# Kernel tuning notes

Measured on AMD Instinct MI355X. Metric: run time of the kernel, lower is better.

## Reference

```python
import jax, jax.numpy as jnp
import numpy as np

B, T_PREFIX, C_IN = 8, 6144, 8
OUT_LEN, OUT_C = 2048, 8
AUX_DIM = 16
D_MODEL, D_STATE, HEADDIM, EXPAND = 256, 32, 64, 2
D_INNER = EXPAND * D_MODEL            # 512
NHEADS = D_INNER // HEADDIM           # 8
CONV_DIM = D_INNER + 2 * D_STATE      # 576
D_PROJ = 2 * D_INNER + 2 * D_STATE + NHEADS  # 1096
N_LAYERS = 2
CHUNK = 64
PATCH = 16
PRECONV_K = 5
DCONV_K = 4


def setup_inputs() -> dict:
    key = jax.random.key(0)
    ks = iter(jax.random.split(key, 64))
    def rn(shape, s=0.02):
        return s * jax.random.normal(next(ks), shape, jnp.float32)
    inp = dict(
        x_prefix=jax.random.normal(next(ks), (B, T_PREFIX, C_IN), jnp.float32),
        y_aux=jax.random.normal(next(ks), (B, AUX_DIM), jnp.float32),
        pre_conv_w=rn((D_MODEL, C_IN, PRECONV_K), 0.1),
        pre_conv_b=rn((D_MODEL,)),
        patch_w=rn((D_MODEL, D_MODEL, PATCH), 0.05),
        patch_b=rn((D_MODEL,)),
        mask_token=rn((D_MODEL,)),
        aux_w=rn((AUX_DIM, D_MODEL), 0.1),
        aux_b=rn((D_MODEL,)),
        patch_out_w=rn((2 * D_MODEL, OUT_C * PATCH), 0.05),
        patch_out_b=rn((OUT_C * PATCH,)),
    )
    for d in ('fwd', 'bwd'):
        inp[f'{d}_norm_w'] = jnp.ones((N_LAYERS, D_MODEL), jnp.float32)
        inp[f'{d}_inproj'] = rn((N_LAYERS, D_MODEL, D_PROJ), 0.05)
        inp[f'{d}_conv_w'] = rn((N_LAYERS, CONV_DIM, DCONV_K), 0.2)
        inp[f'{d}_conv_b'] = rn((N_LAYERS, CONV_DIM))
        inp[f'{d}_dtbias'] = rn((N_LAYERS, NHEADS), 0.5)
        inp[f'{d}_Alog'] = jnp.tile(jnp.log(jnp.arange(1, NHEADS + 1, dtype=jnp.float32)), (N_LAYERS, 1))
        inp[f'{d}_D'] = jnp.ones((N_LAYERS, NHEADS), jnp.float32)
        inp[f'{d}_gnorm'] = jnp.ones((N_LAYERS, D_INNER), jnp.float32)
        inp[f'{d}_outproj'] = rn((N_LAYERS, D_INNER, D_MODEL), 0.05)
    return inp


def rmsnorm(x, w, eps=1e-5):
    return x * jax.lax.rsqrt(jnp.mean(x * x, axis=-1, keepdims=True) + eps) * w


def conv1d(x, w, b, stride, pad):  # x: [B,C,T], w: [O,I,K]
    y = jax.lax.conv_general_dilated(x, w, (stride,), [(pad, pad)],
                                     dimension_numbers=('NCH', 'OIH', 'NCH'))
    return y + b[None, :, None]


def mamba_block(u, inproj, conv_w, conv_b, dtbias, Alog, Dp, gnorm_w, outproj):
    # Mamba-2/SSD style block: in_proj -> z | xBC | dt, causal depthwise conv,
    # selective scan with per-head scalar decay A, +D skip, gated RMSNorm, out_proj.
    b, T, _ = u.shape
    zxbcdt = u @ inproj                                   # [b,T,D_PROJ]
    z = zxbcdt[..., :D_INNER]
    xBC = zxbcdt[..., D_INNER:D_INNER + CONV_DIM]
    dt = jax.nn.softplus(zxbcdt[..., -NHEADS:] + dtbias)  # [b,T,H]
    # causal depthwise conv over time
    xc = jax.lax.conv_general_dilated(xBC.transpose(0, 2, 1), conv_w[:, None, :], (1,),
                                      [(DCONV_K - 1, 0)],
                                      dimension_numbers=('NCH', 'OIH', 'NCH'),
                                      feature_group_count=CONV_DIM)
    xBC = jax.nn.silu((xc + conv_b[None, :, None]).transpose(0, 2, 1))
    xs = xBC[..., :D_INNER].reshape(b, T, NHEADS, HEADDIM)  # [b,T,H,P]
    Bm = xBC[..., D_INNER:D_INNER + D_STATE]                # [b,T,N]
    Cm = xBC[..., D_INNER + D_STATE:]                       # [b,T,N]
    A = -jnp.exp(Alog)                                      # [H]

    def step(h, inps):  # h: [b,H,P,N]
        dt_t, x_t, B_t, C_t = inps
        dA = jnp.exp(dt_t * A)[:, :, None, None]
        h = h * dA + (dt_t[:, :, None] * x_t)[..., None] * B_t[:, None, None, :]
        y = jnp.einsum('bhpn,bn->bhp', h, C_t)
        return h, y

    h0 = jnp.zeros((b, NHEADS, HEADDIM, D_STATE), u.dtype)
    _, ys = jax.lax.scan(step, h0, (dt.transpose(1, 0, 2), xs.transpose(1, 0, 2, 3),
                                    Bm.transpose(1, 0, 2), Cm.transpose(1, 0, 2)))
    y = ys.transpose(1, 0, 2, 3) + Dp[None, None, :, None] * xs
    y = y.reshape(b, T, D_INNER)
    y = rmsnorm(y * jax.nn.silu(z), gnorm_w)
    return y @ outproj


def reference(x_prefix, y_aux, pre_conv_w, pre_conv_b, patch_w, patch_b, mask_token,
              aux_w, aux_b, fwd_norm_w, fwd_inproj, fwd_conv_w, fwd_conv_b, fwd_dtbias,
              fwd_Alog, fwd_D, fwd_gnorm, fwd_outproj, bwd_norm_w, bwd_inproj,
              bwd_conv_w, bwd_conv_b, bwd_dtbias, bwd_Alog, bwd_D, bwd_gnorm,
              bwd_outproj, patch_out_w, patch_out_b):
    b = x_prefix.shape[0]
    t_total = T_PREFIX + OUT_LEN
    x_full = jnp.pad(x_prefix, ((0, 0), (0, OUT_LEN), (0, 0)))        # zeros for future
    x = jax.nn.silu(conv1d(x_full.transpose(0, 2, 1), pre_conv_w, pre_conv_b, 1, PRECONV_K // 2))
    x = conv1d(x, patch_w, patch_b, PATCH, 0).transpose(0, 2, 1)      # [b, n_tokens, d_model]
    n_tokens = x.shape[1]
    # eval mode: deterministic future-patch mask, dropout is identity
    starts = jnp.arange(n_tokens) * PATCH
    mask = (starts >= T_PREFIX)[None, :, None]
    x = jnp.where(mask, mask_token[None, None, :], x)
    aux_bias = jax.nn.silu(y_aux @ aux_w + aux_b)[:, None, :]
    x = x + aux_bias
    pad_t = (-n_tokens) % CHUNK
    if pad_t:
        x = jnp.pad(x, ((0, 0), (0, pad_t), (0, 0)))
    h_f = x
    h_b = x[:, ::-1]
    for i in range(N_LAYERS):
        h_f = h_f + mamba_block(rmsnorm(h_f, fwd_norm_w[i]), fwd_inproj[i], fwd_conv_w[i],
                                fwd_conv_b[i], fwd_dtbias[i], fwd_Alog[i], fwd_D[i],
                                fwd_gnorm[i], fwd_outproj[i])
        h_b = h_b + mamba_block(rmsnorm(h_b, bwd_norm_w[i]), bwd_inproj[i], bwd_conv_w[i],
                                bwd_conv_b[i], bwd_dtbias[i], bwd_Alog[i], bwd_D[i],
                                bwd_gnorm[i], bwd_outproj[i])
    h = jnp.concatenate([h_f, h_b[:, ::-1]], axis=-1)[:, :n_tokens]   # [b,n,2*d_model]
    patch_pred = h @ patch_out_w + patch_out_b                        # [b,n,out_c*patch]
    y = patch_pred.reshape(b, n_tokens, OUT_C, PATCH).reshape(b, n_tokens * PATCH, OUT_C)
    y = y[:, :t_total, :]
    return y[:, T_PREFIX:, :]
```

## Files before the change

### kernel.cpp

```cpp
#include <hip/hip_runtime.h>
#include <hip/hip_bf16.h>
#include <math.h>

#define BSZ      8
#define TPREF    6144
#define CIN      8
#define DMODEL   256
#define DINNER   512
#define DSTATE   32
#define NHEADS   8
#define HEADDIM  64
#define CONVDIM  576
#define DPROJ    1096
#define NTOK     512
#define NVIS     384
#define TBWD     128
#define MFWD     (BSZ * NTOK)
#define MBWD     (BSZ * TBWD)
#define MALL     (MFWD + MBWD)

typedef float f32x4 __attribute__((ext_vector_type(4)));
typedef __bf16 bf16x8 __attribute__((ext_vector_type(8)));

__device__ __forceinline__ float silu_f(float x) { return x / (1.f + expf(-x)); }
// ... 26 lines not shown
        #pragma unroll
        for (int i = 0; i < 2; i++) {
            int s = i * 256 + tid;
            ASYNC16(A + (size_t)(m0 + (s >> 2)) * K + kb + (s & 3) * 8, sm + s * 16);
        }
        #pragma unroll
        for (int i = 0; i < 2; i++) {
            int s = i * 256 + tid;
            ASYNC16(Bt + (size_t)(n0 + (s >> 2)) * K + kb + (s & 3) * 8, sm + 8192 + s * 16);
        }
        __syncthreads();
        bf16x8 af[4], bfr[4];
        #pragma unroll
        for (int mf = 0; mf < 4; mf++)
            af[mf] = *(const bf16x8*)(sm + (wm * 64 + mf * 16 + lm) * 64 + q * 16);
        #pragma unroll
        for (int nf = 0; nf < 4; nf++)
            bfr[nf] = *(const bf16x8*)(sm + 8192 + (wn * 64 + nf * 16 + lm) * 64 + q * 16);
        #pragma unroll
        for (int mf = 0; mf < 4; mf++)
            #pragma unroll
            for (int nf = 0; nf < 4; nf++)
                acc[mf][nf] = __builtin_amdgcn_mfma_f32_16x16x32_bf16(af[mf], bfr[nf], acc[mf][nf], 0, 0, 0);
        __syncthreads();
    }

    #pragma unroll
    for (int mf = 0; mf < 4; mf++) {
        int mbase = m0 + wm * 64 + mf * 16 + q * 4;
        #pragma unroll
        for (int nf = 0; nf < 4; nf++) {
            int n = n0 + wn * 64 + nf * 16 + lm;
            if (n < N) {
                #pragma unroll
                for (int r = 0; r < 4; r++) {
                    float v = acc[mf][nf][r];
                    size_t ci = (size_t)(mbase + r) * ldc + n;
                    if (flags & 4) {
                        v = silu_f(v + bias[n]);
                        ((__bf16*)C)[ci] = (__bf16)v;
                    } else if (flags & 8) {
                        C[ci + (size_t)blockIdx.z * pstr] = v;
                    } else if (flags & 2) {
                        atomicAdd(C + ci, v);
                    } else {
                        C[ci] = v;
                    }
                }
            }
        }
    }
}

__global__ __launch_bounds__(256) void gemm_inproj_norm(
    const float* __restrict__ h, const float* __restrict__ wnf, const float* __restrict__ wnb,
    const __bf16* __restrict__ ipTf, const __bf16* __restrict__ ipTb,
    float* __restrict__ C) {
    __shared__ __bf16 Asm[128][264];
    __shared__ char Bsm[8192];
    int tid = threadIdx.x;
    int m0 = blockIdx.y * 128, n0 = blockIdx.x * 128;
    int dir = (m0 >= MFWD);
    const float* wnorm = dir ? wnb : wnf;
    const __bf16* Bt = dir ? ipTb : ipTf;
    {
        int row = tid >> 1, half = tid & 1;
        const float4* xr = (const float4*)(h + (size_t)(m0 + row) * 256 + half * 128);
        const float4* wr = (const float4*)(wnorm + half * 128);
        float ss = 0.f;
        #pragma unroll
        for (int c = 0; c < 32; c++) {
            float4 v = xr[c], wv = wr[c];
            ss += v.x * v.x + v.y * v.y + v.z * v.z + v.w * v.w;
            __bf16 t4b[4] = {(__bf16)(v.x * wv.x), (__bf16)(v.y * wv.y),
                             (__bf16)(v.z * wv.z), (__bf16)(v.w * wv.w)};
            *(uint2*)&Asm[row][half * 128 + c * 4] = *(uint2*)t4b;
        }
        ss += __shfl_xor(ss, 1);
        float rs = rsqrtf(ss * (1.f / 256.f) + 1e-5f);
        #pragma unroll
        for (int c = 0; c < 16; c++) {
            union { uint4 u; __bf16 hh[8]; } a;
            a.u = *(uint4*)&Asm[row][half * 128 + c * 8];
            #pragma unroll
            for (int j = 0; j < 8; j++) a.hh[j] = (__bf16)((float)a.hh[j] * rs);
            *(uint4*)&Asm[row][half * 128 + c * 8] = a.u;
        }
    }
    __syncthreads();
    int w = tid >> 6, l = tid & 63;
    int wm = w >> 1, wn_ = w & 1, lm = l & 15, q = l >> 4;
    f32x4 acc[4][4];
    #pragma unroll
    for (int i = 0; i < 4; i++)
        #pragma unroll
        for (int j = 0; j < 4; j++) acc[i][j] = (f32x4)0.f;
    for (int k0 = 0; k0 < 256; k0 += 32) {
        #pragma unroll
        for (int i = 0; i < 2; i++) {
            int s = i * 256 + tid;
            ASYNC16(Bt + (size_t)(n0 + (s >> 2)) * 256 + k0 + (s & 3) * 8, Bsm + s * 16);
        }
        __syncthreads();
        bf16x8 af[4], bfr[4];
        #pragma unroll
        for (int mf = 0; mf < 4; mf++)
            af[mf] = *(const bf16x8*)&Asm[wm * 64 + mf * 16 + lm][k0 + q * 8];
        #pragma unroll
        for (int nf = 0; nf < 4; nf++)
            bfr[nf] = *(const bf16x8*)(Bsm + (wn_ * 64 + nf * 16 + lm) * 64 + q * 16);
        #pragma unroll
        for (int mf = 0; mf < 4; mf++)
            #pragma unroll
            for (int nf = 0; nf < 4; nf++)
                acc[mf][nf] = __builtin_amdgcn_mfma_f32_16x16x32_bf16(af[mf], bfr[nf], acc[mf][nf], 0, 0, 0);
        __syncthreads();
    }
    #pragma unroll
    for (int mf = 0; mf < 4; mf++) {
        int mbase = m0 + wm * 64 + mf * 16 + q * 4;
        #pragma unroll
        for (int nf = 0; nf < 4; nf++) {
            int n = n0 + wn_ * 64 + nf * 16 + lm;
            if (n < DPROJ) {
                #pragma unroll
                for (int r = 0; r < 4; r++)
                    C[(size_t)(mbase + r) * DPROJ + n] = acc[mf][nf][r];
            }
        }
    }
}

__global__ __launch_bounds__(256) void gemm_outproj_gated(
    const __bf16* __restrict__ ysD, const float* __restrict__ zx,
    const float* __restrict__ gwf, const float* __restrict__ gwb,
    const __bf16* __restrict__ opTf, const __bf16* __restrict__ opTb,
    float* __restrict__ C) {
    __shared__ __bf16 Asm[64][520];
    __shared__ char Bsm[8192];
    int tid = threadIdx.x;
    int m0 = blockIdx.y * 64, n0 = blockIdx.x * 128;
    int dir = (m0 >= MFWD);
    const float* gw = dir ? gwb : gwf;
    const __bf16* Bt = dir ? opTb : opTf;
    {
        int row = tid >> 2, part = tid & 3;
        size_t gm = m0 + row;
        const uint4* yr = (const uint4*)(ysD + gm * 512 + part * 128);
        const float4* zr = (const float4*)(zx + gm * DPROJ + part * 128);
        const float4* gr = (const float4*)(gw + part * 128);
        float ss = 0.f;
        #pragma unroll
        for (int c = 0; c < 16; c++) {
            union { uint4 u; __bf16 hh[8]; } yv; yv.u = yr[c];
            float4 z0 = zr[c * 2], z1 = zr[c * 2 + 1];
            float4 g0 = gr[c * 2], g1 = gr[c * 2 + 1];
            float gg[8];
            gg[0] = (float)yv.hh[0] * silu_f(z0.x);
            gg[1] = (float)yv.hh[1] * silu_f(z0.y);
            gg[2] = (float)yv.hh[2] * silu_f(z0.z);
            gg[3] = (float)yv.hh[3] * silu_f(z0.w);
            gg[4] = (float)yv.hh[4] * silu_f(z1.x);
            gg[5] = (float)yv.hh[5] * silu_f(z1.y);
            gg[6] = (float)yv.hh[6] * silu_f(z1.z);
            gg[7] = (float)yv.hh[7] * silu_f(z1.w);
            #pragma unroll
            for (int j = 0; j < 8; j++) ss += gg[j] * gg[j];
            union { uint4 u; __bf16 hh[8]; } d;
            d.hh[0] = (__bf16)(gg[0] * g0.x); d.hh[1] = (__bf16)(gg[1] * g0.y);
            d.hh[2] = (__bf16)(gg[2] * g0.z); d.hh[3] = (__bf16)(gg[3] * g0.w);
            d.hh[4] = (__bf16)(gg[4] * g1.x); d.hh[5] = (__bf16)(gg[5] * g1.y);
            d.hh[6] = (__bf16)(gg[6] * g1.z); d.hh[7] = (__bf16)(gg[7] * g1.w);
            *(uint4*)&Asm[row][part * 128 + c * 8] = d.u;
        }
        ss += __shfl_xor(ss, 1);
        ss += __shfl_xor(ss, 2);
        float rs = rsqrtf(ss * (1.f / 512.f) + 1e-5f);
        #pragma unroll
        for (int c = 0; c < 16; c++) {
            union { uint4 u; __bf16 hh[8]; } a;
            a.u = *(uint4*)&Asm[row][part * 128 + c * 8];
            #pragma unroll
            for (int j = 0; j < 8; j++) a.hh[j] = (__bf16)((float)a.hh[j] * rs);
            *(uint4*)&Asm[row][part * 128 + c * 8] = a.u;
        }
    }
    __syncthreads();
    int w = tid >> 6, l = tid & 63;
    int wm = w >> 1, wn_ = w & 1, lm = l & 15, q = l >> 4;
    f32x4 acc[2][4];
    #pragma unroll
    for (int i = 0; i < 2; i++)
        #pragma unroll
        for (int j = 0; j < 4; j++) acc[i][j] = (f32x4)0.f;
    for (int k0 = 0; k0 < 512; k0 += 32) {
        #pragma unroll
        for (int i = 0; i < 2; i++) {
            int s = i * 256 + tid;
            ASYNC16(Bt + (size_t)(n0 + (s >> 2)) * 512 + k0 + (s & 3) * 8, Bsm + s * 16);
        }
        __syncthreads();
        bf16x8 af[2], bfr[4];
        #pragma unroll
        for (int mf = 0; mf < 2; mf++)
            af[mf] = *(const bf16x8*)&Asm[wm * 32 + mf * 16 + lm][k0 + q * 8];
        #pragma unroll
        for (int nf = 0; nf < 4; nf++)
            bfr[nf] = *(const bf16x8*)(Bsm + (wn_ * 64 + nf * 16 + lm) * 64 + q * 16);
        #pragma unroll
        for (int mf = 0; mf < 2; mf++)
            #pragma unroll
            for (int nf = 0; nf < 4; nf++)
                acc[mf][nf] = __builtin_amdgcn_mfma_f32_16x16x32_bf16(af[mf], bfr[nf], acc[mf][nf], 0, 0, 0);
        __syncthreads();
    }
    #pragma unroll
    for (int mf = 0; mf < 2; mf++) {
        int mbase = m0 + wm * 32 + mf * 16 + q * 4;
        #pragma unroll
        for (int nf = 0; nf < 4; nf++) {
            int n = n0 + wn_ * 64 + nf * 16 + lm;
            #pragma unroll
            for (int r = 0; r < 4; r++) {
                size_t ci = (size_t)(mbase + r) * DMODEL + n;
                C[ci] += acc[mf][nf][r];
            }
        }
    }
}

__global__ void prep_all(const float* __restrict__ pre_conv_w, const float* __restrict__ patch_w,
                         const float* __restrict__ ip0, const float* __restrict__ ip1,
                         const float* __restrict__ op0, const float* __restrict__ op1,
                         const float* __restrict__ pow_, const float* __restrict__ pob,
                         const float* __restrict__ y_aux, const float* __restrict__ aux_w,
                         const float* __restrict__ aux_b, const float* __restrict__ xp,
                         __bf16* __restrict__ WpreT, __bf16* __restrict__ WtT,
                         __bf16* __restrict__ inprojT, __bf16* __restrict__ outprojT,
                         __bf16* __restrict__ poT, float* __restrict__ auxb,
                         float* __restrict__ dout, __bf16* __restrict__ Aim) {
    __shared__ float tile[32][33];
    int bx = blockIdx.x, tid = threadIdx.x;
    int tx = tid & 31, ty = tid >> 5;
    if (bx < 256) {
        int o = bx, c = tid;
        float f[16];
        const float4* s = (const float4*)(patch_w + (size_t)o * 4096 + c * 16);
        #pragma unroll
        for (int j = 0; j < 4; j++) *(float4*)&f[j * 4] = s[j];
        #pragma unroll
        for (int k = 0; k < 16; k++)
            WtT[(size_t)o * 4096 + k * 256 + c] = (__bf16)f[k];
        return;
    }
    bx -= 256;
    if (bx < 1152) {
        int seg = bx / 288, rem = bx % 288;
        int n0 = (rem / 8) * 32, k0 = (rem % 8) * 32;
        const float* src = (seg < 2 ? ip0 : ip1) + (size_t)(seg & 1) * 256 * DPROJ;
        #pragma unroll
        for (int j = 0; j < 4; j++) {
            int r = ty + j * 8;
            int n = n0 + tx;
            tile[r][tx] = (n < DPROJ) ? src[(size_t)(k0 + r) * DPROJ + n] : 0.f;
        }
        __syncthreads();
        __bf16* dst = inprojT + (size_t)seg * 1152 * 256;
        #pragma unroll
        for (int j = 0; j < 4; j++) {
            int r = ty + j * 8;
            dst[(size_t)(n0 + r) * 256 + k0 + tx] = (__bf16)tile[tx][r];
        }
        return;
    }
    bx -= 1152;
    if (bx < 512) {
        int s = bx / 128, rem = bx % 128;
        int n0 = (rem / 16) * 32, k0 = (rem % 16) * 32;
        const float* src = (s < 2 ? op0 : op1) + (size_t)(s & 1) * DINNER * DMODEL;
        #pragma unroll
        for (int j = 0; j < 4; j++) {
// ... 92 lines not shown
__global__ __launch_bounds__(256) void dwconv2_kernel(
    const float* __restrict__ zx, const float* __restrict__ cwf, const float* __restrict__ cbf,
    const float* __restrict__ cwb, const float* __restrict__ cbb,
    __bf16* __restrict__ XtF, __bf16* __restrict__ XtB,
    __bf16* __restrict__ BCF, __bf16* __restrict__ BCB) {
    int cg = blockIdx.x;
    int id = blockIdx.y;
    int b, t0, T; size_t rowbase;
    const float *cw, *cb; __bf16 *Xt, *BC;
    if (id < 64) { b = id >> 3; t0 = (id & 7) * 64; T = NTOK; rowbase = (size_t)b * NTOK;
                   cw = cwf; cb = cbf; Xt = XtF; BC = BCF; }
    else { int i2 = id - 64; b = i2 >> 1; t0 = (i2 & 1) * 64; T = TBWD;
           rowbase = (size_t)MFWD + (size_t)b * TBWD; cw = cwb; cb = cbb; Xt = XtB; BC = BCB; }
    int c0 = cg * 64;
    __shared__ float xs[67][65];
    int lane = threadIdx.x & 63, grp = threadIdx.x >> 6;
    for (int r = grp; r < 67; r += 4) {
        int t = t0 - 3 + r;
        xs[r][lane] = (t >= 0) ? zx[(rowbase + t) * DPROJ + DINNER + c0 + lane] : 0.f;
    }
    __syncthreads();
    if (cg < 8) {
        int t = lane;
        #pragma unroll
        for (int ci = grp; ci < 64; ci += 4) {
            int c = c0 + ci;
            float acc = cb[c];
            #pragma unroll
            for (int k = 0; k < 4; k++) acc += cw[c * 4 + k] * xs[t + k][ci];
            Xt[((size_t)((b * 8 + cg) * 64 + ci)) * T + t0 + t] = (__bf16)silu_f(acc);
        }
    } else {
        int c = lane;
        #pragma unroll
        for (int ti = grp; ti < 64; ti += 4) {
            float acc = cb[c0 + c];
            #pragma unroll
            for (int k = 0; k < 4; k++) acc += cw[(c0 + c) * 4 + k] * xs[ti + k][c];
            BC[((size_t)(b * T + t0 + ti)) * 64 + c] = (__bf16)silu_f(acc);
        }
    }
}

__global__ __launch_bounds__(64) void scan_local(
    const __bf16* __restrict__ XtF, const __bf16* __restrict__ XtB,
    const __bf16* __restrict__ BCF, const __bf16* __restrict__ BCB,
    const float* __restrict__ zx,
    const float* __restrict__ dtbf, const float* __restrict__ dtbb,
    const float* __restrict__ Alogf, const float* __restrict__ Alogb,
    const float* __restrict__ Dpf, const float* __restrict__ Dpb,
    __bf16* __restrict__ ysD,
    __bf16* __restrict__ ChatF, __bf16* __restrict__ ChatB,
    float* __restrict__ dSF, float* __restrict__ dSB,
    float* __restrict__ DcsF, float* __restrict__ DcsB) {
    int id = blockIdx.x, hd = blockIdx.y;
    int b, c, T, NC; size_t rowbase;
    const __bf16 *Xt, *BC; __bf16* Chat; float *dS, *Dcs;
    const float *dtb, *Alog, *Dp;
    if (id < 64) { b = id >> 3; c = id & 7; T = NTOK; NC = 8; rowbase = (size_t)b * NTOK;
                   Xt = XtF; BC = BCF; Chat = ChatF; dS = dSF; Dcs = DcsF;
                   dtb = dtbf; Alog = Alogf; Dp = Dpf; }
    else { int i2 = id - 64; b = i2 >> 1; c = i2 & 1; T = TBWD; NC = 2;
           rowbase = (size_t)MFWD + (size_t)b * TBWD;
           Xt = XtB; BC = BCB; Chat = ChatB; dS = dSB; Dcs = DcsB;
           dtb = dtbb; Alog = Alogb; Dp = Dpb; }
    int bh = b * 8 + hd;
    int t0 = c * 64;
    int lane = threadIdx.x;
    int lm = lane & 15, q = lane >> 4;
    float A = -expf(Alog[hd]);
    float Dh = Dp[hd];

    __shared__ __bf16 Xl[64][72];
    __shared__ __bf16 BCl[64][72];
    __shared__ __bf16 Pl[64][72];
    __shared__ __bf16 Wbl[32][72];
    __shared__ float lcs[64], dts[64];

    const uint4* xg = (const uint4*)(Xt + (size_t)(bh * 64 + lane) * T + t0);
    const uint4* bg = (const uint4*)(BC + ((size_t)(b * T + t0 + lane)) * 64);
    uint4 xv[8], bv[8];
    #pragma unroll
    for (int k = 0; k < 8; k++) { xv[k] = xg[k]; bv[k] = bg[k]; }
    float xdt = zx[(rowbase + t0 + lane) * DPROJ + 1088 + hd] + dtb[hd];
    float dtv = (xdt > 20.f) ? xdt : log1pf(expf(xdt));
    #pragma unroll
    for (int k = 0; k < 8; k++) {
        *(uint4*)&Xl[lane][k * 8] = xv[k];
        *(uint4*)&BCl[lane][k * 8] = bv[k];
    }
    float lc = A * dtv;
    #pragma unroll
    for (int off = 1; off < 64; off <<= 1) {
        float o = __shfl_up(lc, off);
        if (lane >= off) lc += o;
    }
    lcs[lane] = lc; dts[lane] = dtv;
    float lc63 = __shfl(lc, 63);
    float wj = expf(lc63 - lc) * dtv;
    float eli = expf(lc);
    float Dc = expf(lc63);
    if (lane == 0) Dcs[bh * NC + c] = Dc;
    {
        __bf16* co = Chat + ((size_t)(bh * NC + c) * 64 + lane) * 32;
        #pragma unroll
        for (int k = 0; k < 4; k++) {
            union { uint4 u; __bf16 h[8]; } s; s.u = bv[4 + k];
            union { uint4 u; __bf16 h[8]; } d;
            #pragma unroll
            for (int j = 0; j < 8; j++) d.h[j] = (__bf16)(eli * (float)s.h[j]);
            *(uint4*)(co + k * 8) = d.u;
        }
    }
    #pragma unroll
    for (int k = 0; k < 4; k++) {
        union { uint4 u; __bf16 h[8]; } s; s.u = bv[k];
        #pragma unroll
        for (int j = 0; j < 8; j++) Wbl[k * 8 + j][lane] = (__bf16)(wj * (float)s.h[j]);
    }
    __syncthreads();

    bf16x8 cfr[4], bfr[4];
    #pragma unroll
    for (int t4 = 0; t4 < 4; t4++) {
        cfr[t4] = *(const bf16x8*)&BCl[t4 * 16 + lm][32 + q * 8];
        bfr[t4] = *(const bf16x8*)&BCl[t4 * 16 + lm][q * 8];
    }
    #pragma unroll
    for (int ti = 0; ti < 4; ti++) {
        float lci[4];
        #pragma unroll
        for (int r = 0; r < 4; r++) lci[r] = lcs[ti * 16 + q * 4 + r];
        #pragma unroll
        for (int tj = 0; tj < 4; tj++) {
            if (tj > ti) {
                #pragma unroll
                for (int r = 0; r < 4; r++) Pl[ti * 16 + q * 4 + r][tj * 16 + lm] = (__bf16)0.f;
                continue;
            }
            f32x4 g = __builtin_amdgcn_mfma_f32_16x16x32_bf16(cfr[ti], bfr[tj], (f32x4)0.f, 0, 0, 0);
            int j = tj * 16 + lm;
            float lcj = lcs[j], dtj = dts[j];
            #pragma unroll
            for (int r = 0; r < 4; r++) {
                int i = ti * 16 + q * 4 + r;
                float v = (j <= i) ? g[r] * expf(lci[r] - lcj) * dtj : 0.f;
                if (j == i) v += Dh;
                Pl[i][j] = (__bf16)v;
            }
        }
    }
    __syncthreads();

    bf16x8 pf0[4], pf1[4], xf0[4], xf1[4];
    #pragma unroll
    for (int t4 = 0; t4 < 4; t4++) {
        pf0[t4] = *(const bf16x8*)&Pl[t4 * 16 + lm][q * 8];
        pf1[t4] = *(const bf16x8*)&Pl[t4 * 16 + lm][32 + q * 8];
        xf0[t4] = *(const bf16x8*)&Xl[t4 * 16 + lm][q * 8];
        xf1[t4] = *(const bf16x8*)&Xl[t4 * 16 + lm][32 + q * 8];
    }
    #pragma unroll
    for (int ti = 0; ti < 4; ti++) {
        #pragma unroll
        for (int tp = 0; tp < 4; tp++) {
            f32x4 y = __builtin_amdgcn_mfma_f32_16x16x32_bf16(pf0[ti], xf0[tp], (f32x4)0.f, 0, 0, 0);
            y = __builtin_amdgcn_mfma_f32_16x16x32_bf16(pf1[ti], xf1[tp], y, 0, 0, 0);
            #pragma unroll
            for (int r = 0; r < 4; r++) {
                int i = ti * 16 + q * 4 + r;
                ysD[(rowbase + t0 + i) * DINNER + hd * 64 + tp * 16 + lm] = (__bf16)y[r];
            }
        }
    }
    bf16x8 wf0[2], wf1[2];
    #pragma unroll
    for (int tn = 0; tn < 2; tn++) {
        wf0[tn] = *(const bf16x8*)&Wbl[tn * 16 + lm][q * 8];
        wf1[tn] = *(const bf16x8*)&Wbl[tn * 16 + lm][32 + q * 8];
    }
    float* dso = dS + (size_t)(bh * NC + c) * 2048;
    #pragma unroll
    for (int tp = 0; tp < 4; tp++) {
        #pragma unroll
        for (int tn = 0; tn < 2; tn++) {
            f32x4 s = __builtin_amdgcn_mfma_f32_16x16x32_bf16(xf0[tp], wf0[tn], (f32x4)0.f, 0, 0, 0);
            s = __builtin_amdgcn_mfma_f32_16x16x32_bf16(xf1[tp], wf1[tn], s, 0, 0, 0);
            #pragma unroll
            for (int r = 0; r < 4; r++) {
                int pp = tp * 16 + q * 4 + r, nn = tn * 16 + lm;
                dso[pp * 32 + nn] = s[r];
            }
        }
    }
}

__global__ __launch_bounds__(256) void scan_tail(
    const float* __restrict__ dSF, const float* __restrict__ dSB,
    const float* __restrict__ DcsF, const float* __restrict__ DcsB,
    const __bf16* __restrict__ ChatF, const __bf16* __restrict__ ChatB,
    __bf16* __restrict__ ysD) {
    int blk = blockIdx.x;
    int dir = blk >= 64;
    int bh = blk & 63;
    int NC = dir ? 2 : 8;
    int T = dir ? TBWD : NTOK;
    int b = bh >> 3, hd = bh & 7;
    size_t rowbase = dir ? ((size_t)MFWD + (size_t)b * TBWD) : ((size_t)b * NTOK);
    const float* dS = dir ? dSB : dSF;
    const float* Dcs = dir ? DcsB : DcsF;
    const __bf16* Chat = dir ? ChatB : ChatF;
    int tid = threadIdx.x;
    __shared__ __bf16 Spl[8][64][40];
    {
        int p = tid >> 2, n0 = (tid & 3) * 8;
        float S[8];
        #pragma unroll
        for (int j = 0; j < 8; j++) S[j] = 0.f;
        for (int c = 0; c < NC; c++) {
            union { uint4 u; __bf16 hh[8]; } o;
            #pragma unroll
            for (int j = 0; j < 8; j++) o.hh[j] = (__bf16)S[j];
            *(uint4*)&Spl[c][p][n0] = o.u;
            float Dc = Dcs[bh * NC + c];
            const float4* dp = (const float4*)(dS + ((size_t)(bh * NC + c)) * 2048 + tid * 8);
            float4 d0 = dp[0], d1 = dp[1];
            S[0] = Dc * S[0] + d0.x; S[1] = Dc * S[1] + d0.y;
            S[2] = Dc * S[2] + d0.z; S[3] = Dc * S[3] + d0.w;
            S[4] = Dc * S[4] + d1.x; S[5] = Dc * S[5] + d1.y;
            S[6] = Dc * S[6] + d1.z; S[7] = Dc * S[7] + d1.w;
        }
    }
    __syncthreads();
    int w = tid >> 6, l = tid & 63, lm = l & 15, q = l >> 4;
    for (int c = 1 + w; c < NC; c += 4) {
        int t0 = c * 64;
        const __bf16* Cb = Chat + (size_t)(bh * NC + c) * 2048;
        bf16x8 cf[4], sf[4];
        #pragma unroll
        for (int t4 = 0; t4 < 4; t4++) {
            cf[t4] = *(const bf16x8*)(Cb + (t4 * 16 + lm) * 32 + q * 8);
            sf[t4] = *(const bf16x8*)&Spl[c][t4 * 16 + lm][q * 8];
        }
        #pragma unroll
        for (int ti = 0; ti < 4; ti++) {
            #pragma unroll
            for (int tp = 0; tp < 4; tp++) {
                f32x4 y = __builtin_amdgcn_mfma_f32_16x16x32_bf16(cf[ti], sf[tp], (f32x4)0.f, 0, 0, 0);
                #pragma unroll
                for (int r = 0; r < 4; r++) {
                    int i = ti * 16 + q * 4 + r;
                    size_t idx = (rowbase + t0 + i) * DINNER + hd * 64 + tp * 16 + lm;
                    ysD[idx] = (__bf16)((float)ysD[idx] + y[r]);
                }
            }
        }
    }
}

__global__ void hcat_kernel(const float* __restrict__ h_all, __bf16* __restrict__ hc) {
    int idx = blockIdx.x * 256 + threadIdx.x;
    if (idx >= BSZ * TBWD * DINNER) return;
    int c = idx & 511, j = (idx >> 9) & 127, b = idx >> 16;
    float v = (c < 256) ? h_all[(size_t)(b * NTOK + NVIS + j) * 256 + c]
                        : h_all[(size_t)MFWD * 256 + (size_t)(b * TBWD + (TBWD - 1 - j)) * 256 + (c - 256)];
    hc[idx] = (__bf16)v;
}

extern "C" void kernel_launch(void* const* d_in, const int* in_sizes, int n_in,
                              void* d_out, int out_size, void* d_ws, size_t ws_size,
                              hipStream_t stream) {
    const float* x_prefix    = (const float*)d_in[0];
    const float* y_aux       = (const float*)d_in[1];
    const float* pre_conv_w  = (const float*)d_in[2];
    const float* pre_conv_b  = (const float*)d_in[3];
    const float* patch_w     = (const float*)d_in[4];
    const float* patch_b     = (const float*)d_in[5];
    const float* mask_token  = (const float*)d_in[6];
    const float* aux_w       = (const float*)d_in[7];
    const float* aux_b       = (const float*)d_in[8];
    const float* patch_out_w = (const float*)d_in[9];
    const float* patch_out_b = (const float*)d_in[10];
    const float* w_norm[2]   = {(const float*)d_in[11], (const float*)d_in[20]};
    const float* w_inproj[2] = {(const float*)d_in[12], (const float*)d_in[21]};
    const float* w_convw[2]  = {(const float*)d_in[13], (const float*)d_in[22]};
    const float* w_convb[2]  = {(const float*)d_in[14], (const float*)d_in[23]};
    const float* w_dtb[2]    = {(const float*)d_in[15], (const float*)d_in[24]};
    const float* w_alog[2]   = {(const float*)d_in[16], (const float*)d_in[25]};
    const float* w_D[2]      = {(const float*)d_in[17], (const float*)d_in[26]};
    const float* w_gnorm[2]  = {(const float*)d_in[18], (const float*)d_in[27]};
    const float* w_outproj[2]= {(const float*)d_in[19], (const float*)d_in[28]};

    char* p = (char*)d_ws;
    auto alloc = [&](size_t bytes) { char* r = p; p += (bytes + 255) & ~255ULL; return r; };
    __bf16* A_patch  = (__bf16*)alloc((size_t)3072 * 4096 * 2);
    __bf16* Aim      = (__bf16*)alloc((size_t)BSZ * TPREF * 64 * 2);
    __bf16* WpreT    = (__bf16*)alloc((size_t)256 * 64 * 2);
    __bf16* WtT      = (__bf16*)alloc((size_t)256 * 4096 * 2);
    __bf16* inprojT  = (__bf16*)alloc((size_t)4 * 1152 * 256 * 2);
    __bf16* outprojT = (__bf16*)alloc((size_t)4 * 256 * 512 * 2);
    __bf16* poT      = (__bf16*)alloc((size_t)128 * 512 * 2);
    float*  auxb     = (float*)alloc(8 * 256 * 4);
    float*  Cp4      = (float*)alloc((size_t)4 * 3072 * 256 * 4);
    float*  h_all    = (float*)alloc((size_t)MALL * 256 * 4);
    float*  zx       = (float*)alloc((size_t)MALL * DPROJ * 4);
    __bf16* XtF      = (__bf16*)alloc((size_t)64 * 64 * NTOK * 2);
    __bf16* XtB      = (__bf16*)alloc((size_t)64 * 64 * TBWD * 2);
    __bf16* BCF      = (__bf16*)alloc((size_t)BSZ * NTOK * 64 * 2);
    __bf16* BCB      = (__bf16*)alloc((size_t)BSZ * TBWD * 64 * 2);
    __bf16* ysD      = (__bf16*)alloc((size_t)MALL * DINNER * 2);
    __bf16* hct      = (__bf16*)alloc((size_t)1024 * DINNER * 2);
    __bf16* ChatF    = (__bf16*)alloc((size_t)64 * 8 * 2048 * 2);
    __bf16* ChatB    = (__bf16*)alloc((size_t)64 * 2 * 2048 * 2);
    float*  dSF      = (float*)alloc((size_t)64 * 8 * 2048 * 4);
    float*  dSB      = (float*)alloc((size_t)64 * 2 * 2048 * 4);
    float*  DcsF     = (float*)alloc((size_t)64 * 8 * 4);
    float*  DcsB     = (float*)alloc((size_t)64 * 2 * 4);

    prep_all<<<256 + 1152 + 512 + 64 + 64 + 512 + 192 + 8, 256, 0, stream>>>(
        pre_conv_w, patch_w, w_inproj[0], w_inproj[1], w_outproj[0], w_outproj[1],
        patch_out_w, patch_out_b, y_aux, aux_w, aux_b, x_prefix,
        WpreT, WtT, inprojT, outprojT, poT, auxb, (float*)d_out, Aim);
    gemm_mfma<<<dim3(2, (BSZ * TPREF) / 128, 1), 256, 0, stream>>>(
        Aim, WpreT, (float*)A_patch, pre_conv_b, 256, 64, 256, 4, 0);
    gemm_mfma<<<dim3(2, 24, 4), 256, 0, stream>>>(
        A_patch, WtT, Cp4, nullptr, 256, 4096, 256, 8, (long)3072 * 256);
    assemble_kernel<<<(BSZ * NTOK * DMODEL) / 256, 256, 0, stream>>>(
        Cp4, patch_b, mask_token, auxb, h_all);

    for (int i = 0; i < 2; i++) {
        const __bf16* ipTf = inprojT + (size_t)(0 * 2 + i) * 1152 * 256;
        const __bf16* ipTb = inprojT + (size_t)(1 * 2 + i) * 1152 * 256;
        const __bf16* opTf = outprojT + (size_t)(0 * 2 + i) * 256 * 512;
        const __bf16* opTb = outprojT + (size_t)(1 * 2 + i) * 256 * 512;
        gemm_inproj_norm<<<dim3(9, MALL / 128), 256, 0, stream>>>(
            h_all, w_norm[0] + i * 256, w_norm[1] + i * 256, ipTf, ipTb, zx);
        dwconv2_kernel<<<dim3(9, 80), 256, 0, stream>>>(
            zx, w_convw[0] + i * CONVDIM * 4, w_convb[0] + i * CONVDIM,
            w_convw[1] + i * CONVDIM * 4, w_convb[1] + i * CONVDIM,
            XtF, XtB, BCF, BCB);
        scan_local<<<dim3(80, NHEADS), 64, 0, stream>>>(
            XtF, XtB, BCF, BCB, zx,
            w_dtb[0] + i * 8, w_dtb[1] + i * 8,
            w_alog[0] + i * 8, w_alog[1] + i * 8,
            w_D[0] + i * 8, w_D[1] + i * 8,
            ysD, ChatF, ChatB, dSF, dSB, DcsF, DcsB);
        scan_tail<<<128, 256, 0, stream>>>(dSF, dSB, DcsF, DcsB, ChatF, ChatB, ysD);
        gemm_outproj_gated<<<dim3(2, MALL / 64), 256, 0, stream>>>(
            ysD, zx, w_gnorm[0] + i * DINNER, w_gnorm[1] + i * DINNER, opTf, opTb, h_all);
    }

    hcat_kernel<<<(BSZ * TBWD * DINNER) / 256, 256, 0, stream>>>(h_all, hct);
    gemm_mfma<<<dim3(1, 8, 4), 256, 0, stream>>>(
        hct, poT, (float*)d_out, nullptr, 128, 512, 128, 2, 0);
}
```

Before: 381.1 us.

## Split norms out of projection GEMMs and skip unused forward rows in final layer

RMSNorm and the gated norm move out of the in/out projection GEMMs into standalone row kernels that write bf16 activations. Both GEMMs then stream A and B tiles through async copies with 128x128 tiles. In the last layer, the forward direction only computes intra-chunk outputs, tail corrections and out-projection rows for the chunks that reach the final output, which avoids dead work on visible-prefix tokens. This adds two extra launches and an extra bf16 round trip through global memory for the normalized activations.

```diff
diff --git a/kernel.cpp b/kernel.cpp
--- a/kernel.cpp
+++ b/kernel.cpp
@@ -102,44 +102,15 @@
     }
 }
 
-__global__ __launch_bounds__(256) void gemm_inproj_norm(
-    const float* __restrict__ h, const float* __restrict__ wnf, const float* __restrict__ wnb,
-    const __bf16* __restrict__ ipTf, const __bf16* __restrict__ ipTb,
-    float* __restrict__ C) {
-    __shared__ __bf16 Asm[128][264];
-    __shared__ char Bsm[8192];
+__global__ __launch_bounds__(256) void gemm_inproj(
+    const __bf16* __restrict__ u, const __bf16* __restrict__ ipTf,
+    const __bf16* __restrict__ ipTb, float* __restrict__ C) {
+    __shared__ char sm[16384];
     int tid = threadIdx.x;
     int m0 = blockIdx.y * 128, n0 = blockIdx.x * 128;
-    int dir = (m0 >= MFWD);
-    const float* wnorm = dir ? wnb : wnf;
-    const __bf16* Bt = dir ? ipTb : ipTf;
-    {
-        int row = tid >> 1, half = tid & 1;
-        const float4* xr = (const float4*)(h + (size_t)(m0 + row) * 256 + half * 128);
-        const float4* wr = (const float4*)(wnorm + half * 128);
-        float ss = 0.f;
-        #pragma unroll
-        for (int c = 0; c < 32; c++) {
-            float4 v = xr[c], wv = wr[c];
-            ss += v.x * v.x + v.y * v.y + v.z * v.z + v.w * v.w;
-            __bf16 t4b[4] = {(__bf16)(v.x * wv.x), (__bf16)(v.y * wv.y),
-                             (__bf16)(v.z * wv.z), (__bf16)(v.w * wv.w)};
-            *(uint2*)&Asm[row][half * 128 + c * 4] = *(uint2*)t4b;
-        }
-        ss += __shfl_xor(ss, 1);
-        float rs = rsqrtf(ss * (1.f / 256.f) + 1e-5f);
-        #pragma unroll
-        for (int c = 0; c < 16; c++) {
-            union { uint4 u; __bf16 hh[8]; } a;
-            a.u = *(uint4*)&Asm[row][half * 128 + c * 8];
-            #pragma unroll
-            for (int j = 0; j < 8; j++) a.hh[j] = (__bf16)((float)a.hh[j] * rs);
-            *(uint4*)&Asm[row][half * 128 + c * 8] = a.u;
-        }
-    }
-    __syncthreads();
+    const __bf16* Bt = (m0 >= MFWD) ? ipTb : ipTf;
     int w = tid >> 6, l = tid & 63;
-    int wm = w >> 1, wn_ = w & 1, lm = l & 15, q = l >> 4;
+    int wm = w >> 1, wn = w & 1, lm = l & 15, q = l >> 4;
     f32x4 acc[4][4];
     #pragma unroll
     for (int i = 0; i < 4; i++)
@@ -149,16 +120,21 @@
         #pragma unroll
         for (int i = 0; i < 2; i++) {
             int s = i * 256 + tid;
-            ASYNC16(Bt + (size_t)(n0 + (s >> 2)) * 256 + k0 + (s & 3) * 8, Bsm + s * 16);
+            ASYNC16(u + (size_t)(m0 + (s >> 2)) * 256 + k0 + (s & 3) * 8, sm + s * 16);
+        }
+        #pragma unroll
+        for (int i = 0; i < 2; i++) {
+            int s = i * 256 + tid;
+            ASYNC16(Bt + (size_t)(n0 + (s >> 2)) * 256 + k0 + (s & 3) * 8, sm + 8192 + s * 16);
         }
         __syncthreads();
         bf16x8 af[4], bfr[4];
         #pragma unroll
         for (int mf = 0; mf < 4; mf++)
-            af[mf] = *(const bf16x8*)&Asm[wm * 64 + mf * 16 + lm][k0 + q * 8];
+            af[mf] = *(const bf16x8*)(sm + (wm * 64 + mf * 16 + lm) * 64 + q * 16);
         #pragma unroll
         for (int nf = 0; nf < 4; nf++)
-            bfr[nf] = *(const bf16x8*)(Bsm + (wn_ * 64 + nf * 16 + lm) * 64 + q * 16);
+            bfr[nf] = *(const bf16x8*)(sm + 8192 + (wn * 64 + nf * 16 + lm) * 64 + q * 16);
         #pragma unroll
         for (int mf = 0; mf < 4; mf++)
             #pragma unroll
@@ -171,7 +147,7 @@
         int mbase = m0 + wm * 64 + mf * 16 + q * 4;
         #pragma unroll
         for (int nf = 0; nf < 4; nf++) {
-            int n = n0 + wn_ * 64 + nf * 16 + lm;
+            int n = n0 + wn * 64 + nf * 16 + lm;
             if (n < DPROJ) {
                 #pragma unroll
                 for (int r = 0; r < 4; r++)
@@ -181,95 +157,55 @@
     }
 }
 
-__global__ __launch_bounds__(256) void gemm_outproj_gated(
-    const __bf16* __restrict__ ysD, const float* __restrict__ zx,
-    const float* __restrict__ gwf, const float* __restrict__ gwb,
-    const __bf16* __restrict__ opTf, const __bf16* __restrict__ opTb,
-    float* __restrict__ C) {
-    __shared__ __bf16 Asm[64][520];
-    __shared__ char Bsm[8192];
+__global__ __launch_bounds__(256) void gemm_outproj(
+    const __bf16* __restrict__ y2, const __bf16* __restrict__ opTf,
+    const __bf16* __restrict__ opTb, float* __restrict__ C, int layer) {
+    __shared__ char sm[16384];
     int tid = threadIdx.x;
-    int m0 = blockIdx.y * 64, n0 = blockIdx.x * 128;
-    int dir = (m0 >= MFWD);
-    const float* gw = dir ? gwb : gwf;
-    const __bf16* Bt = dir ? opTb : opTf;
-    {
-        int row = tid >> 2, part = tid & 3;
-        size_t gm = m0 + row;
-        const uint4* yr = (const uint4*)(ysD + gm * 512 + part * 128);
-        const float4* zr = (const float4*)(zx + gm * DPROJ + part * 128);
-        const float4* gr = (const float4*)(gw + part * 128);
-        float ss = 0.f;
-        #pragma unroll
-        for (int c = 0; c < 16; c++) {
-            union { uint4 u; __bf16 hh[8]; } yv; yv.u = yr[c];
-            float4 z0 = zr[c * 2], z1 = zr[c * 2 + 1];
-            float4 g0 = gr[c * 2], g1 = gr[c * 2 + 1];
-            float gg[8];
-            gg[0] = (float)yv.hh[0] * silu_f(z0.x);
-            gg[1] = (float)yv.hh[1] * silu_f(z0.y);
-            gg[2] = (float)yv.hh[2] * silu_f(z0.z);
-            gg[3] = (float)yv.hh[3] * silu_f(z0.w);
-            gg[4] = (float)yv.hh[4] * silu_f(z1.x);
-            gg[5] = (float)yv.hh[5] * silu_f(z1.y);
-            gg[6] = (float)yv.hh[6] * silu_f(z1.z);
-            gg[7] = (float)yv.hh[7] * silu_f(z1.w);
-            #pragma unroll
-            for (int j = 0; j < 8; j++) ss += gg[j] * gg[j];
-            union { uint4 u; __bf16 hh[8]; } d;
-            d.hh[0] = (__bf16)(gg[0] * g0.x); d.hh[1] = (__bf16)(gg[1] * g0.y);
-            d.hh[2] = (__bf16)(gg[2] * g0.z); d.hh[3] = (__bf16)(gg[3] * g0.w);
-            d.hh[4] = (__bf16)(gg[4] * g1.x); d.hh[5] = (__bf16)(gg[5] * g1.y);
-            d.hh[6] = (__bf16)(gg[6] * g1.z); d.hh[7] = (__bf16)(gg[7] * g1.w);
-            *(uint4*)&Asm[row][part * 128 + c * 8] = d.u;
-        }
-        ss += __shfl_xor(ss, 1);
-        ss += __shfl_xor(ss, 2);
-        float rs = rsqrtf(ss * (1.f / 512.f) + 1e-5f);
-        #pragma unroll
-        for (int c = 0; c < 16; c++) {
-            union { uint4 u; __bf16 hh[8]; } a;
-            a.u = *(uint4*)&Asm[row][part * 128 + c * 8];
-            #pragma unroll
-            for (int j = 0; j < 8; j++) a.hh[j] = (__bf16)((float)a.hh[j] * rs);
-            *(uint4*)&Asm[row][part * 128 + c * 8] = a.u;
-        }
-    }
-    __syncthreads();
+    int yb = blockIdx.y;
+    int m0 = (layer == 0) ? yb * 128
+                          : ((yb < 8) ? (yb * 512 + 384) : (MFWD + (yb - 8) * 128));
+    int n0 = blockIdx.x * 128;
+    const __bf16* Bt = (m0 >= MFWD) ? opTb : opTf;
     int w = tid >> 6, l = tid & 63;
-    int wm = w >> 1, wn_ = w & 1, lm = l & 15, q = l >> 4;
-    f32x4 acc[2][4];
-    #pragma unroll
-    for (int i = 0; i < 2; i++)
+    int wm = w >> 1, wn = w & 1, lm = l & 15, q = l >> 4;
+    f32x4 acc[4][4];
+    #pragma unroll
+    for (int i = 0; i < 4; i++)
         #pragma unroll
         for (int j = 0; j < 4; j++) acc[i][j] = (f32x4)0.f;
     for (int k0 = 0; k0 < 512; k0 += 32) {
         #pragma unroll
         for (int i = 0; i < 2; i++) {
             int s = i * 256 + tid;
-            ASYNC16(Bt + (size_t)(n0 + (s >> 2)) * 512 + k0 + (s & 3) * 8, Bsm + s * 16);
-        }
-        __syncthreads();
-        bf16x8 af[2], bfr[4];
-        #pragma unroll
-        for (int mf = 0; mf < 2; mf++)
-            af[mf] = *(const bf16x8*)&Asm[wm * 32 + mf * 16 + lm][k0 + q * 8];
+            ASYNC16(y2 + (size_t)(m0 + (s >> 2)) * 512 + k0 + (s & 3) * 8, sm + s * 16);
+        }
+        #pragma unroll
+        for (int i = 0; i < 2; i++) {
+            int s = i * 256 + tid;
+            ASYNC16(Bt + (size_t)(n0 + (s >> 2)) * 512 + k0 + (s & 3) * 8, sm + 8192 + s * 16);
+        }
+        __syncthreads();
+        bf16x8 af[4], bfr[4];
+        #pragma unroll
+        for (int mf = 0; mf < 4; mf++)
+            af[mf] = *(const bf16x8*)(sm + (wm * 64 + mf * 16 + lm) * 64 + q * 16);
         #pragma unroll
         for (int nf = 0; nf < 4; nf++)
-            bfr[nf] = *(const bf16x8*)(Bsm + (wn_ * 64 + nf * 16 + lm) * 64 + q * 16);
-        #pragma unroll
-        for (int mf = 0; mf < 2; mf++)
+            bfr[nf] = *(const bf16x8*)(sm + 8192 + (wn * 64 + nf * 16 + lm) * 64 + q * 16);
+        #pragma unroll
+        for (int mf = 0; mf < 4; mf++)
             #pragma unroll
             for (int nf = 0; nf < 4; nf++)
                 acc[mf][nf] = __builtin_amdgcn_mfma_f32_16x16x32_bf16(af[mf], bfr[nf], acc[mf][nf], 0, 0, 0);
         __syncthreads();
     }
     #pragma unroll
-    for (int mf = 0; mf < 2; mf++) {
-        int mbase = m0 + wm * 32 + mf * 16 + q * 4;
+    for (int mf = 0; mf < 4; mf++) {
+        int mbase = m0 + wm * 64 + mf * 16 + q * 4;
         #pragma unroll
         for (int nf = 0; nf < 4; nf++) {
-            int n = n0 + wn_ * 64 + nf * 16 + lm;
+            int n = n0 + wn * 64 + nf * 16 + lm;
             #pragma unroll
             for (int r = 0; r < 4; r++) {
                 size_t ci = (size_t)(mbase + r) * DMODEL + n;
@@ -277,6 +213,55 @@
             }
         }
     }
+}
+
+__global__ __launch_bounds__(256) void rmsnorm_all(
+    const float* __restrict__ h, const float* __restrict__ wf,
+    const float* __restrict__ wb, __bf16* __restrict__ u) {
+    int row = blockIdx.x * 4 + (threadIdx.x >> 6);
+    int lane = threadIdx.x & 63;
+    const float* w = (row >= MFWD) ? wb : wf;
+    float4 v = ((const float4*)(h + (size_t)row * 256))[lane];
+    float ss = v.x * v.x + v.y * v.y + v.z * v.z + v.w * v.w;
+    #pragma unroll
+    for (int off = 32; off >= 1; off >>= 1) ss += __shfl_xor(ss, off);
+    float rs = rsqrtf(ss * (1.f / 256.f) + 1e-5f);
+    float4 wv = ((const float4*)w)[lane];
+    __bf16 o4[4] = {(__bf16)(v.x * rs * wv.x), (__bf16)(v.y * rs * wv.y),
+                    (__bf16)(v.z * rs * wv.z), (__bf16)(v.w * rs * wv.w)};
+    *(uint2*)(u + (size_t)row * 256 + lane * 4) = *(uint2*)o4;
+}
+
+__global__ __launch_bounds__(256) void gatednorm_all(
+    const __bf16* __restrict__ ysD, const float* __restrict__ zx,
+    const float* __restrict__ gwf, const float* __restrict__ gwb,
+    __bf16* __restrict__ y2) {
+    int row = blockIdx.x * 4 + (threadIdx.x >> 6);
+    int lane = threadIdx.x & 63;
+    const float* gw = (row >= MFWD) ? gwb : gwf;
+    union { uint4 u; __bf16 hh[8]; } yv;
+    yv.u = *(const uint4*)(ysD + (size_t)row * 512 + lane * 8);
+    const float4* zr = (const float4*)(zx + (size_t)row * DPROJ + lane * 8);
+    float4 z0 = zr[0], z1 = zr[1];
+    float g[8];
+    g[0] = (float)yv.hh[0] * silu_f(z0.x); g[1] = (float)yv.hh[1] * silu_f(z0.y);
+    g[2] = (float)yv.hh[2] * silu_f(z0.z); g[3] = (float)yv.hh[3] * silu_f(z0.w);
+    g[4] = (float)yv.hh[4] * silu_f(z1.x); g[5] = (float)yv.hh[5] * silu_f(z1.y);
+    g[6] = (float)yv.hh[6] * silu_f(z1.z); g[7] = (float)yv.hh[7] * silu_f(z1.w);
+    float ss = 0.f;
+    #pragma unroll
+    for (int j = 0; j < 8; j++) ss += g[j] * g[j];
+    #pragma unroll
+    for (int off = 32; off >= 1; off >>= 1) ss += __shfl_xor(ss, off);
+    float rs = rsqrtf(ss * (1.f / 512.f) + 1e-5f);
+    const float4* gr = (const float4*)(gw + lane * 8);
+    float4 g0 = gr[0], g1 = gr[1];
+    union { uint4 u; __bf16 hh[8]; } d;
+    d.hh[0] = (__bf16)(g[0] * rs * g0.x); d.hh[1] = (__bf16)(g[1] * rs * g0.y);
+    d.hh[2] = (__bf16)(g[2] * rs * g0.z); d.hh[3] = (__bf16)(g[3] * rs * g0.w);
+    d.hh[4] = (__bf16)(g[4] * rs * g1.x); d.hh[5] = (__bf16)(g[5] * rs * g1.y);
+    d.hh[6] = (__bf16)(g[6] * rs * g1.z); d.hh[7] = (__bf16)(g[7] * rs * g1.w);
+    *(uint4*)(y2 + (size_t)row * 512 + lane * 8) = d.u;
 }
 
 __global__ void prep_all(const float* __restrict__ pre_conv_w, const float* __restrict__ patch_w,
@@ -475,7 +460,7 @@
     __bf16* __restrict__ ysD,
     __bf16* __restrict__ ChatF, __bf16* __restrict__ ChatB,
     float* __restrict__ dSF, float* __restrict__ dSB,
-    float* __restrict__ DcsF, float* __restrict__ DcsB) {
+    float* __restrict__ DcsF, float* __restrict__ DcsB, int layer) {
     int id = blockIdx.x, hd = blockIdx.y;
     int b, c, T, NC; size_t rowbase;
     const __bf16 *Xt, *BC; __bf16* Chat; float *dS, *Dcs;
@@ -487,6 +472,7 @@
            rowbase = (size_t)MFWD + (size_t)b * TBWD;
            Xt = XtB; BC = BCB; Chat = ChatB; dS = dSB; Dcs = DcsB;
            dtb = dtbb; Alog = Alogb; Dp = Dpb; }
+    bool skipY = (layer == 1) && (id < 64) && (c < 6);
     int bh = b * 8 + hd;
     int t0 = c * 64;
     int lane = threadIdx.x;
@@ -494,11 +480,13 @@
     float A = -expf(Alog[hd]);
     float Dh = Dp[hd];
 
-    __shared__ __bf16 Xl[64][72];
-    __shared__ __bf16 BCl[64][72];
-    __shared__ __bf16 Pl[64][72];
-    __shared__ __bf16 Wbl[32][72];
-    __shared__ float lcs[64], dts[64];
+    __shared__ char smem[23552];
+    __bf16 (*Xl)[72]  = (__bf16(*)[72])(smem);
+    __bf16 (*BCl)[72] = (__bf16(*)[72])(smem + 9216);
+    __bf16 (*Pl)[72]  = (__bf16(*)[72])(smem + 9216);
+    __bf16 (*Wbl)[72] = (__bf16(*)[72])(smem + 18432);
+    float* lcs = (float*)(smem + 23040);
+    float* dts = (float*)(smem + 23296);
 
     const uint4* xg = (const uint4*)(Xt + (size_t)(bh * 64 + lane) * T + t0);
     const uint4* bg = (const uint4*)(BC + ((size_t)(b * T + t0 + lane)) * 64);
@@ -510,7 +498,7 @@
     #pragma unroll
     for (int k = 0; k < 8; k++) {
         *(uint4*)&Xl[lane][k * 8] = xv[k];
-        *(uint4*)&BCl[lane][k * 8] = bv[k];
+        if (!skipY) *(uint4*)&BCl[lane][k * 8] = bv[k];
     }
     float lc = A * dtv;
     #pragma unroll
@@ -524,7 +512,7 @@
     float eli = expf(lc);
     float Dc = expf(lc63);
     if (lane == 0) Dcs[bh * NC + c] = Dc;
-    {
+    if (!skipY) {
         __bf16* co = Chat + ((size_t)(bh * NC + c) * 64 + lane) * 32;
         #pragma unroll
         for (int k = 0; k < 4; k++) {
@@ -543,57 +531,66 @@
     }
     __syncthreads();
 
-    bf16x8 cfr[4], bfr[4];
-    #pragma unroll
-    for (int t4 = 0; t4 < 4; t4++) {
-        cfr[t4] = *(const bf16x8*)&BCl[t4 * 16 + lm][32 + q * 8];
-        bfr[t4] = *(const bf16x8*)&BCl[t4 * 16 + lm][q * 8];
-    }
-    #pragma unroll
-    for (int ti = 0; ti < 4; ti++) {
-        float lci[4];
-        #pragma unroll
-        for (int r = 0; r < 4; r++) lci[r] = lcs[ti * 16 + q * 4 + r];
-        #pragma unroll
-        for (int tj = 0; tj < 4; tj++) {
-            if (tj > ti) {
+    bf16x8 xf0[4], xf1[4];
+    if (!skipY) {
+        bf16x8 cfr[4], bfr[4];
+        #pragma unroll
+        for (int t4 = 0; t4 < 4; t4++) {
+            cfr[t4] = *(const bf16x8*)&BCl[t4 * 16 + lm][32 + q * 8];
+            bfr[t4] = *(const bf16x8*)&BCl[t4 * 16 + lm][q * 8];
+        }
+        #pragma unroll
+        for (int ti = 0; ti < 4; ti++) {
+            float lci[4];
+            #pragma unroll
+            for (int r = 0; r < 4; r++) lci[r] = lcs[ti * 16 + q * 4 + r];
+            #pragma unroll
+            for (int tj = 0; tj < 4; tj++) {
+                if (tj > ti) {
+                    #pragma unroll
+                    for (int r = 0; r < 4; r++) Pl[ti * 16 + q * 4 + r][tj * 16 + lm] = (__bf16)0.f;
+                    continue;
+                }
+                f32x4 g = __builtin_amdgcn_mfma_f32_16x16x32_bf16(cfr[ti], bfr[tj], (f32x4)0.f, 0, 0, 0);
+                int j = tj * 16 + lm;
+                float lcj = lcs[j], dtj = dts[j];
                 #pragma unroll
-                for (int r = 0; r < 4; r++) Pl[ti * 16 + q * 4 + r][tj * 16 + lm] = (__bf16)0.f;
-                continue;
+                for (int r = 0; r < 4; r++) {
+                    int i = ti * 16 + q * 4 + r;
+                    float v = (j <= i) ? g[r] * expf(lci[r] - lcj) * dtj : 0.f;
+                    if (j == i) v += Dh;
+                    Pl[i][j] = (__bf16)v;
+                }
             }
-            f32x4 g = __builtin_amdgcn_mfma_f32_16x16x32_bf16(cfr[ti], bfr[tj], (f32x4)0.f, 0, 0, 0);
-            int j = tj * 16 + lm;
-            float lcj = lcs[j], dtj = dts[j];
-            #pragma unroll
-            for (int r = 0; r < 4; r++) {
-                int i = ti * 16 + q * 4 + r;
-                float v = (j <= i) ? g[r] * expf(lci[r] - lcj) * dtj : 0.f;
-                if (j == i) v += Dh;
-                Pl[i][j] = (__bf16)v;
+        }
+        __syncthreads();
+
+        bf16x8 pf0[4], pf1[4];
+        #pragma unroll
+        for (int t4 = 0; t4 < 4; t4++) {
+            pf0[t4] = *(const bf16x8*)&Pl[t4 * 16 + lm][q * 8];
+            pf1[t4] = *(const bf16x8*)&Pl[t4 * 16 + lm][32 + q * 8];
+            xf0[t4] = *(const bf16x8*)&Xl[t4 * 16 + lm][q * 8];
+            xf1[t4] = *(const bf16x8*)&Xl[t4 * 16 + lm][32 + q * 8];
+        }
+        #pragma unroll
+        for (int ti = 0; ti < 4; ti++) {
+            #pragma unroll
+            for (int tp = 0; tp < 4; tp++) {
+                f32x4 y = __builtin_amdgcn_mfma_f32_16x16x32_bf16(pf0[ti], xf0[tp], (f32x4)0.f, 0, 0, 0);
+                y = __builtin_amdgcn_mfma_f32_16x16x32_bf16(pf1[ti], xf1[tp], y, 0, 0, 0);
+                #pragma unroll
+                for (int r = 0; r < 4; r++) {
+                    int i = ti * 16 + q * 4 + r;
+                    ysD[(rowbase + t0 + i) * DINNER + hd * 64 + tp * 16 + lm] = (__bf16)y[r];
+                }
             }
         }
-    }
-    __syncthreads();
-
-    bf16x8 pf0[4], pf1[4], xf0[4], xf1[4];
-    #pragma unroll
-    for (int t4 = 0; t4 < 4; t4++) {
-        pf0[t4] = *(const bf16x8*)&Pl[t4 * 16 + lm][q * 8];
-        pf1[t4] = *(const bf16x8*)&Pl[t4 * 16 + lm][32 + q * 8];
-        xf0[t4] = *(const bf16x8*)&Xl[t4 * 16 + lm][q * 8];
-        xf1[t4] = *(const bf16x8*)&Xl[t4 * 16 + lm][32 + q * 8];
-    }
-    #pragma unroll
-    for (int ti = 0; ti < 4; ti++) {
-        #pragma unroll
-        for (int tp = 0; tp < 4; tp++) {
-            f32x4 y = __builtin_amdgcn_mfma_f32_16x16x32_bf16(pf0[ti], xf0[tp], (f32x4)0.f, 0, 0, 0);
-            y = __builtin_amdgcn_mfma_f32_16x16x32_bf16(pf1[ti], xf1[tp], y, 0, 0, 0);
-            #pragma unroll
-            for (int r = 0; r < 4; r++) {
-                int i = ti * 16 + q * 4 + r;
-                ysD[(rowbase + t0 + i) * DINNER + hd * 64 + tp * 16 + lm] = (__bf16)y[r];
-            }
+    } else {
+        #pragma unroll
+        for (int t4 = 0; t4 < 4; t4++) {
+            xf0[t4] = *(const bf16x8*)&Xl[t4 * 16 + lm][q * 8];
+            xf1[t4] = *(const bf16x8*)&Xl[t4 * 16 + lm][32 + q * 8];
         }
     }
     bf16x8 wf0[2], wf1[2];
@@ -622,7 +619,7 @@
     const float* __restrict__ dSF, const float* __restrict__ dSB,
     const float* __restrict__ DcsF, const float* __restrict__ DcsB,
     const __bf16* __restrict__ ChatF, const __bf16* __restrict__ ChatB,
-    __bf16* __restrict__ ysD) {
+    __bf16* __restrict__ ysD, int layer) {
     int blk = blockIdx.x;
     int dir = blk >= 64;
     int bh = blk & 63;
@@ -633,6 +630,7 @@
     const float* dS = dir ? dSB : dSF;
     const float* Dcs = dir ? DcsB : DcsF;
     const __bf16* Chat = dir ? ChatB : ChatF;
+    int cmin = (layer == 1 && !dir) ? 6 : 1;
     int tid = threadIdx.x;
     __shared__ __bf16 Spl[8][64][40];
     {
@@ -656,7 +654,7 @@
     }
     __syncthreads();
     int w = tid >> 6, l = tid & 63, lm = l & 15, q = l >> 4;
-    for (int c = 1 + w; c < NC; c += 4) {
+    for (int c = cmin + w; c < NC; c += 4) {
         int t0 = c * 64;
         const __bf16* Cb = Chat + (size_t)(bh * NC + c) * 2048;
         bf16x8 cf[4], sf[4];
@@ -726,12 +724,14 @@
     float*  auxb     = (float*)alloc(8 * 256 * 4);
     float*  Cp4      = (float*)alloc((size_t)4 * 3072 * 256 * 4);
     float*  h_all    = (float*)alloc((size_t)MALL * 256 * 4);
+    __bf16* u        = (__bf16*)alloc((size_t)MALL * 256 * 2);
     float*  zx       = (float*)alloc((size_t)MALL * DPROJ * 4);
     __bf16* XtF      = (__bf16*)alloc((size_t)64 * 64 * NTOK * 2);
     __bf16* XtB      = (__bf16*)alloc((size_t)64 * 64 * TBWD * 2);
     __bf16* BCF      = (__bf16*)alloc((size_t)BSZ * NTOK * 64 * 2);
     __bf16* BCB      = (__bf16*)alloc((size_t)BSZ * TBWD * 64 * 2);
     __bf16* ysD      = (__bf16*)alloc((size_t)MALL * DINNER * 2);
+    __bf16* y2       = (__bf16*)alloc((size_t)MALL * DINNER * 2);
     __bf16* hct      = (__bf16*)alloc((size_t)1024 * DINNER * 2);
     __bf16* ChatF    = (__bf16*)alloc((size_t)64 * 8 * 2048 * 2);
     __bf16* ChatB    = (__bf16*)alloc((size_t)64 * 2 * 2048 * 2);
@@ -756,8 +756,8 @@
         const __bf16* ipTb = inprojT + (size_t)(1 * 2 + i) * 1152 * 256;
         const __bf16* opTf = outprojT + (size_t)(0 * 2 + i) * 256 * 512;
         const __bf16* opTb = outprojT + (size_t)(1 * 2 + i) * 256 * 512;
-        gemm_inproj_norm<<<dim3(9, MALL / 128), 256, 0, stream>>>(
-            h_all, w_norm[0] + i * 256, w_norm[1] + i * 256, ipTf, ipTb, zx);
+        rmsnorm_all<<<MALL / 4, 256, 0, stream>>>(h_all, w_norm[0] + i * 256, w_norm[1] + i * 256, u);
+        gemm_inproj<<<dim3(9, MALL / 128), 256, 0, stream>>>(u, ipTf, ipTb, zx);
         dwconv2_kernel<<<dim3(9, 80), 256, 0, stream>>>(
             zx, w_convw[0] + i * CONVDIM * 4, w_convb[0] + i * CONVDIM,
             w_convw[1] + i * CONVDIM * 4, w_convb[1] + i * CONVDIM,
@@ -767,10 +767,12 @@
             w_dtb[0] + i * 8, w_dtb[1] + i * 8,
             w_alog[0] + i * 8, w_alog[1] + i * 8,
             w_D[0] + i * 8, w_D[1] + i * 8,
-            ysD, ChatF, ChatB, dSF, dSB, DcsF, DcsB);
-        scan_tail<<<128, 256, 0, stream>>>(dSF, dSB, DcsF, DcsB, ChatF, ChatB, ysD);
-        gemm_outproj_gated<<<dim3(2, MALL / 64), 256, 0, stream>>>(
-            ysD, zx, w_gnorm[0] + i * DINNER, w_gnorm[1] + i * DINNER, opTf, opTb, h_all);
+            ysD, ChatF, ChatB, dSF, dSB, DcsF, DcsB, i);
+        scan_tail<<<128, 256, 0, stream>>>(dSF, dSB, DcsF, DcsB, ChatF, ChatB, ysD, i);
+        gatednorm_all<<<MALL / 4, 256, 0, stream>>>(
+            ysD, zx, w_gnorm[0] + i * DINNER, w_gnorm[1] + i * DINNER, y2);
+        int oy = (i == 0) ? (MALL / 128) : 16;
+        gemm_outproj<<<dim3(2, oy), 256, 0, stream>>>(y2, opTf, opTb, h_all, i);
     }
 
     hcat_kernel<<<(BSZ * TBWD * DINNER) / 256, 256, 0, stream>>>(h_all, hct);
```

Result: faster. 339.6 us (-10.9%).
